# Kernel optimization log

Hardware: AMD Instinct MI355X
Metric: run time of the kernel (lower is better)

Reference implementation:

```python
import jax, jax.numpy as jnp
import numpy as np

B, T, D_IN, D_H, D_P = 256, 512, 256, 512, 512

def _lin(k, out_d, in_d):
    # torch nn.Linear default init: U(-1/sqrt(in_d), 1/sqrt(in_d))
    k1, k2 = jax.random.split(k)
    bound = 1.0 / np.sqrt(in_d)
    W = jax.random.uniform(k1, (out_d, in_d), jnp.float32, -bound, bound)
    b = jax.random.uniform(k2, (out_d,), jnp.float32, -bound, bound)
    return W, b

def setup_inputs() -> dict:
    key = jax.random.key(0)
    ks = jax.random.split(key, 8)
    x = jax.random.normal(ks[0], (B, T, D_IN), jnp.float32)
    # RNNCell params (torch init: U(-1/sqrt(hidden), 1/sqrt(hidden)) for all)
    bh = 1.0 / np.sqrt(D_H)
    k = jax.random.split(ks[1], 4)
    W_ih = jax.random.uniform(k[0], (D_H, D_IN), jnp.float32, -bh, bh)
    b_ih = jax.random.uniform(k[1], (D_H,), jnp.float32, -bh, bh)
    W_hh = jax.random.uniform(k[2], (D_H, D_H), jnp.float32, -bh, bh)
    b_hh = jax.random.uniform(k[3], (D_H,), jnp.float32, -bh, bh)
    W_ip, b_ip = _lin(ks[2], D_P, D_IN)
    W_hp, b_hp = _lin(ks[3], D_P, D_H)
    W_g, b_g = _lin(ks[4], D_P, D_IN + D_H)
    W_r, b_r = _lin(ks[5], D_P, D_P)
    W_o, b_o = _lin(ks[6], D_P, D_P)
    return dict(x=x, W_ih=W_ih, b_ih=b_ih, W_hh=W_hh, b_hh=b_hh,
                W_ip=W_ip, b_ip=b_ip, W_hp=W_hp, b_hp=b_hp,
                W_g=W_g, b_g=b_g, W_r=W_r, b_r=b_r, W_o=W_o, b_o=b_o)

def reference(x, W_ih, b_ih, W_hh, b_hh, W_ip, b_ip, W_hp, b_hp,
              W_g, b_g, W_r, b_r, W_o, b_o):
    batch = x.shape[0]
    # Precompute time-parallel projections of x outside the recurrence.
    x_ih = jnp.einsum('bti,hi->bth', x, W_ih) + b_ih + b_hh   # RNN input term
    x_proj_all = jnp.einsum('bti,pi->btp', x, W_ip) + b_ip
    # gate = sigmoid([x_t, h] @ W_g^T + b_g); split W_g into x-part and h-part
    W_gx, W_gh = W_g[:, :x.shape[-1]], W_g[:, x.shape[-1]:]
    gate_x_all = jnp.einsum('bti,pi->btp', x, W_gx) + b_g

    h0 = jnp.zeros((batch, W_hh.shape[0]), x.dtype)

    def step(h, inputs):
        x_ih_t, x_proj, gate_x = inputs
        h = jnp.tanh(x_ih_t + h @ W_hh.T)                # RNNCell (b_ih+b_hh folded in)
        h_proj = h @ W_hp.T + b_hp
        gate = jax.nn.sigmoid(gate_x + h @ W_gh.T)
        blended = gate * h_proj + (1.0 - gate) * x_proj
        res = blended @ W_r.T + b_r
        out_t = jax.nn.relu(res + blended)
        out_t = out_t @ W_o.T + b_o
        return h, out_t

    xs = (jnp.swapaxes(x_ih, 0, 1),       # (T, B, H)
          jnp.swapaxes(x_proj_all, 0, 1), # (T, B, P)
          jnp.swapaxes(gate_x_all, 0, 1)) # (T, B, P)
    _, outs = jax.lax.scan(step, h0, xs)
    return jnp.swapaxes(outs, 0, 1)       # (B, T, P)
```

## Files before the change

### kernel.cpp

```cpp
#include <hip/hip_runtime.h>
#include <hip/hip_bf16.h>
#include <cstdint>

#define RB   256
#define RT   512
#define ROWS (RB*RT)

typedef __attribute__((ext_vector_type(8))) short bf16x8;
typedef __attribute__((ext_vector_type(4))) short s16x4;
typedef __attribute__((ext_vector_type(4))) float f32x4;

#define DEV static __device__ __forceinline__

DEV float bf2f(unsigned short u){
  union { unsigned int i; float f; } v; v.i = ((unsigned int)u) << 16; return v.f;
}
DEV unsigned short f2bf(float f){
  union { float f; unsigned int i; } v; v.f = f;
  unsigned int x = v.i;
  return (unsigned short)((x + 0x7fffu + ((x >> 16) & 1u)) >> 16);
}
DEV float tanh_fast(float x){
  float xc = fminf(fmaxf(x, -15.f), 15.f);
  float e  = __expf(2.f * xc);
  return 1.f - 2.f * __builtin_amdgcn_rcpf(e + 1.f);
}
DEV float sigmoid_fast(float x){
  float xc = fminf(fmaxf(x, -30.f), 30.f);
  return __builtin_amdgcn_rcpf(1.f + __expf(-xc));
}
DEV void gl_lds16(const void* g, void* l){
  __builtin_amdgcn_global_load_lds(
      (const __attribute__((address_space(1))) unsigned int*)g,
      (__attribute__((address_space(3))) unsigned int*)l, 16, 0, 0);
}

struct ConvArgs {
  const float* src[15];
  unsigned short* dst[15];
  long pre[16];
};

__global__ __launch_bounds__(256) void conv_k(ConvArgs a, long total)
{
  long stride = (long)gridDim.x * blockDim.x;
  for (long idx = (long)blockIdx.x * blockDim.x + threadIdx.x; idx < total; idx += stride){
    int t = 0;
    #pragma unroll
    for (int j = 0; j < 14; j++) t += (idx >= a.pre[j + 1]) ? 1 : 0;
    long local = idx - a.pre[t];
    float4 v = ((const float4*)a.src[t])[local];
    s16x4 o;
    o[0] = (short)f2bf(v.x); o[1] = (short)f2bf(v.y);
    o[2] = (short)f2bf(v.z); o[3] = (short)f2bf(v.w);
    ((s16x4*)a.dst[t])[local] = o;
  }
}

__global__ __launch_bounds__(256, 2) void gemm_k(
    const unsigned short* __restrict__ A, int lda,
    const unsigned short* __restrict__ W, int ldb,
    const unsigned short* __restrict__ bias,
    const unsigned short* __restrict__ bias2,
    const unsigned short* __restrict__ addsrc,
    void* __restrict__ C,
    int K, int act, int out_f32)
{
  __shared__ unsigned short As[128*64];
  __shared__ unsigned short Bs[128*64];
  const int tid = threadIdx.x, w = tid >> 6, l = tid & 63;
  const int wm = w >> 1, wn = w & 1;
  const int lr = l & 15, lk = (l >> 4) * 8;
  const long row0 = (long)blockIdx.x * 128;
  const int  col0 = blockIdx.y * 128;

  f32x4 acc[4][4] = {};

  for (int k0 = 0; k0 < K; k0 += 64){
    __syncthreads();
    #pragma unroll
    for (int i = 0; i < 4; i++){
      int chunk = i*256 + tid;
      int r = chunk >> 3, kc = (chunk & 7) * 8;
      gl_lds16(A + (row0 + r)*lda + k0 + kc, (unsigned short*)As + (i*256 + w*64)*8);
      gl_lds16(W + (long)(col0 + r)*ldb + k0 + kc, (unsigned short*)Bs + (i*256 + w*64)*8);
    }
    asm volatile("s_waitcnt vmcnt(0)" ::: "memory");
    __syncthreads();
    #pragma unroll
    for (int ks = 0; ks < 2; ks++){
      bf16x8 a[4], b[4];
      #pragma unroll
      for (int mt = 0; mt < 4; mt++) a[mt] = *(const bf16x8*)&As[(wm*64 + mt*16 + lr)*64 + ks*32 + lk];
      #pragma unroll
      for (int nt = 0; nt < 4; nt++) b[nt] = *(const bf16x8*)&Bs[(wn*64 + nt*16 + lr)*64 + ks*32 + lk];
      #pragma unroll
      for (int mt = 0; mt < 4; mt++)
        #pragma unroll
        for (int nt = 0; nt < 4; nt++)
          acc[mt][nt] = __builtin_amdgcn_mfma_f32_16x16x32_bf16(a[mt], b[nt], acc[mt][nt], 0, 0, 0);
    }
  }

  #pragma unroll
  for (int nt = 0; nt < 4; nt++){
    int c = col0 + wn*64 + nt*16 + lr;
    float bv = bf2f(bias[c]);
    if (bias2) bv += bf2f(bias2[c]);
    #pragma unroll
    for (int mt = 0; mt < 4; mt++){
      #pragma unroll
      for (int i = 0; i < 4; i++){
        long r = row0 + wm*64 + mt*16 + (l >> 4)*4 + i;
        float v = acc[mt][nt][i] + bv;
        if (addsrc) v += bf2f(addsrc[r*512 + c]);
        if (act) v = fmaxf(v, 0.f);
        if (out_f32) ((float*)C)[r*512 + c] = v;
        else ((unsigned short*)C)[r*512 + c] = f2bf(v);
      }
    }
  }
}

__global__ __launch_bounds__(512, 2) void recur_k(
    const unsigned short* __restrict__ xih,
    const unsigned short* __restrict__ Whh,
    unsigned short* __restrict__ H)
{
  extern __shared__ unsigned short lds[];
  unsigned short* Wl = lds;
  unsigned short* hb = lds + 512*136;

  const int tid = threadIdx.x, w = tid >> 6, l = tid & 63;
  const int lr = l & 15, hi = l >> 4, lk = hi * 8;
  const int b0 = blockIdx.x * 16;
  const int cbase = w * 64;

  #pragma unroll
  for (int i = 0; i < 16; i++){
    int id = i*512 + tid;
    int c = id >> 4, j = (id & 15) * 8;
    *(bf16x8*)&Wl[c*136 + j] = *(const bf16x8*)&Whh[c*512 + 384 + j];
  }
  for (int i = tid; i < 16*520; i += 512) hb[i] = 0;

  bf16x8 wa[4][12];
  #pragma unroll
  for (int nt = 0; nt < 4; nt++){
    int c = cbase + nt*16 + lr;
    #pragma unroll
    for (int ks = 0; ks < 12; ks++)
      wa[nt][ks] = *(const bf16x8*)&Whh[c*512 + ks*32 + lk];
  }
  __syncthreads();

  const long xrow = ((long)(b0 + lr) * RT) * 512;

  for (int t = 0; t < RT; t++){
    uint2 xu[4];
    #pragma unroll
    for (int nt = 0; nt < 4; nt++)
      xu[nt] = *(const uint2*)&xih[xrow + (long)t*512 + cbase + nt*16 + hi*4];

    f32x4 acc[4] = {};
    #pragma unroll
    for (int ks = 0; ks < 16; ks++){
      bf16x8 hf = *(const bf16x8*)&hb[lr*520 + ks*32 + lk];
      #pragma unroll
      for (int nt = 0; nt < 4; nt++){
        bf16x8 af;
        if (ks < 12) af = wa[nt][ks];
        else         af = *(const bf16x8*)&Wl[(cbase + nt*16 + lr)*136 + (ks-12)*32 + lk];
        acc[nt] = __builtin_amdgcn_mfma_f32_16x16x32_bf16(af, hf, acc[nt], 0, 0, 0);
      }
    }

    unsigned int hv[4][2];
    #pragma unroll
    for (int nt = 0; nt < 4; nt++){
      float v0 = tanh_fast(acc[nt][0] + bf2f((unsigned short)(xu[nt].x & 0xffffu)));
      float v1 = tanh_fast(acc[nt][1] + bf2f((unsigned short)(xu[nt].x >> 16)));
      float v2 = tanh_fast(acc[nt][2] + bf2f((unsigned short)(xu[nt].y & 0xffffu)));
      float v3 = tanh_fast(acc[nt][3] + bf2f((unsigned short)(xu[nt].y >> 16)));
      hv[nt][0] = (unsigned)f2bf(v0) | ((unsigned)f2bf(v1) << 16);
      hv[nt][1] = (unsigned)f2bf(v2) | ((unsigned)f2bf(v3) << 16);
    }

    __syncthreads();
    #pragma unroll
    for (int nt = 0; nt < 4; nt++){
      uint2 p; p.x = hv[nt][0]; p.y = hv[nt][1];
      *(uint2*)&hb[lr*520 + cbase + nt*16 + hi*4] = p;
    }
    __syncthreads();

    {
      int r = tid >> 5, cb = (tid & 31) * 16;
      bf16x8 v0 = *(const bf16x8*)&hb[r*520 + cb];
      bf16x8 v1 = *(const bf16x8*)&hb[r*520 + cb + 8];
      long go = ((long)(b0 + r) * RT + t) * 512 + cb;
      *(bf16x8*)&H[go]     = v0;
      *(bf16x8*)&H[go + 8] = v1;
    }
  }
}

__global__ __launch_bounds__(256, 2) void blend_k(
    const unsigned short* __restrict__ X,
    const unsigned short* __restrict__ Hm,
    const unsigned short* __restrict__ Wg,
    const unsigned short* __restrict__ Wip,
    const unsigned short* __restrict__ Whp,
    const unsigned short* __restrict__ bg,
    const unsigned short* __restrict__ bip,
    const unsigned short* __restrict__ bhp,
    unsigned short* __restrict__ Out)
{
  __shared__ unsigned short As[128*64];
  __shared__ unsigned short Gs[128*64];
  __shared__ unsigned short Ps[128*64];
  const int tid = threadIdx.x, w = tid >> 6, l = tid & 63;
  const int wm = w >> 1, wn = w & 1;
  const int lr = l & 15, lk = (l >> 4) * 8;
  const long row0 = (long)blockIdx.x * 128;
  const int  col0 = blockIdx.y * 128;

  f32x4 accg[4][4] = {}, accp[4][4] = {};
  unsigned int xpp[4][4][2];

  #pragma unroll 1
  for (int k0 = 0; k0 < 768; k0 += 64){
    const bool ph1 = (k0 < 256);
    __syncthreads();
    #pragma unroll
    for (int i = 0; i < 4; i++){
      int chunk = i*256 + tid;
      int r = chunk >> 3, kc = (chunk & 7) * 8;
      const unsigned short* asrc = ph1 ? (X  + (row0 + r)*256 + k0 + kc)
                                       : (Hm + (row0 + r)*512 + (k0 - 256) + kc);
      gl_lds16(asrc, (unsigned short*)As + (i*256 + w*64)*8);
      gl_lds16(Wg + (long)(col0 + r)*768 + k0 + kc, (unsigned short*)Gs + (i*256 + w*64)*8);
      const unsigned short* psrc = ph1 ? (Wip + (col0 + r)*256 + k0 + kc)
                                       : (Whp + (col0 + r)*512 + (k0 - 256) + kc);
      gl_lds16(psrc, (unsigned short*)Ps + (i*256 + w*64)*8);
    }
    asm volatile("s_waitcnt vmcnt(0)" ::: "memory");
    __syncthreads();
    #pragma unroll
    for (int ks = 0; ks < 2; ks++){
      bf16x8 a[4], gq[4], pq[4];
      #pragma unroll
      for (int mt = 0; mt < 4; mt++) a[mt]  = *(const bf16x8*)&As[(wm*64 + mt*16 + lr)*64 + ks*32 + lk];
      #pragma unroll
      for (int nt = 0; nt < 4; nt++){
        gq[nt] = *(const bf16x8*)&Gs[(wn*64 + nt*16 + lr)*64 + ks*32 + lk];
        pq[nt] = *(const bf16x8*)&Ps[(wn*64 + nt*16 + lr)*64 + ks*32 + lk];
      }
      #pragma unroll
      for (int mt = 0; mt < 4; mt++)
        #pragma unroll
        for (int nt = 0; nt < 4; nt++){
          accg[mt][nt] = __builtin_amdgcn_mfma_f32_16x16x32_bf16(a[mt], gq[nt], accg[mt][nt], 0, 0, 0);
          accp[mt][nt] = __builtin_amdgcn_mfma_f32_16x16x32_bf16(a[mt], pq[nt], accp[mt][nt], 0, 0, 0);
        }
    }
    if (k0 == 192){
      #pragma unroll
      for (int mt = 0; mt < 4; mt++)
        #pragma unroll
        for (int nt = 0; nt < 4; nt++){
          xpp[mt][nt][0] = (unsigned)f2bf(accp[mt][nt][0]) | ((unsigned)f2bf(accp[mt][nt][1]) << 16);
          xpp[mt][nt][1] = (unsigned)f2bf(accp[mt][nt][2]) | ((unsigned)f2bf(accp[mt][nt][3]) << 16);
          accp[mt][nt] = (f32x4){0.f, 0.f, 0.f, 0.f};
        }
    }
  }

  #pragma unroll
  for (int nt = 0; nt < 4; nt++){
    int c = col0 + wn*64 + nt*16 + lr;
    float bgv = bf2f(bg[c]), bipv = bf2f(bip[c]), bhpv = bf2f(bhp[c]);
    #pragma unroll
    for (int mt = 0; mt < 4; mt++){
      #pragma unroll
      for (int i = 0; i < 4; i++){
        long r = row0 + wm*64 + mt*16 + (l >> 4)*4 + i;
        float g  = sigmoid_fast(accg[mt][nt][i] + bgv);
        float hp = accp[mt][nt][i] + bhpv;
        unsigned u = xpp[mt][nt][i >> 1];
        float xp = bf2f((unsigned short)((i & 1) ? (u >> 16) : (u & 0xffff))) + bipv;
        float v = g * hp + (1.f - g) * xp;
        Out[r*512 + c] = f2bf(v);
      }
    }
  }
}

extern "C" void kernel_launch(void* const* d_in, const int* in_sizes, int n_in,
                              void* d_out, int out_size, void* d_ws, size_t ws_size,
                              hipStream_t stream)
{
  static const long nelem[15] = {
    (long)ROWS*256,
    512*256, 512,
    512*512, 512,
    512*256, 512,
    512*512, 512,
    512*768, 512,
    512*512, 512,
    512*512, 512
  };

  unsigned char* ob = (unsigned char*)d_out;
  unsigned char* wb = (unsigned char*)d_ws;
  ConvArgs ca;
  long pre = 0;
  size_t doff = 0;
  for (int i = 0; i < 15; i++){
    ca.src[i] = (const float*)d_in[i];
    if (i == 13)      ca.dst[i] = (unsigned short*)(wb + 134217728u);
    else if (i == 14) ca.dst[i] = (unsigned short*)(wb + 134742016u);
    else              ca.dst[i] = (unsigned short*)(ob + doff);
    ca.pre[i] = pre;
    pre += nelem[i] / 4;
    if (i == 0) doff = 67108864u;
    else if (i < 13) doff += (size_t)nelem[i] * 2;
  }
  ca.pre[15] = pre;
  const long total_chunks = pre;

  const unsigned short* xb  = ca.dst[0];
  const unsigned short* Wih = ca.dst[1];
  const unsigned short* bih = ca.dst[2];
  const unsigned short* Whh = ca.dst[3];
  const unsigned short* bhh = ca.dst[4];
  const unsigned short* Wip = ca.dst[5];
  const unsigned short* bip = ca.dst[6];
  const unsigned short* Whp = ca.dst[7];
  const unsigned short* bhp = ca.dst[8];
  const unsigned short* Wg  = ca.dst[9];
  const unsigned short* bg  = ca.dst[10];
  const unsigned short* Wr  = ca.dst[11];
  const unsigned short* br  = ca.dst[12];
  const unsigned short* Wo  = ca.dst[13];
  const unsigned short* bo  = ca.dst[14];

  unsigned short* xih  = (unsigned short*)(ob + 75497472u);
  unsigned short* wsb  = (unsigned short*)d_ws;

  dim3 grid(ROWS / 128, 4), block(256);

  conv_k<<<2048, 256, 0, stream>>>(ca, total_chunks);

  gemm_k<<<grid, block, 0, stream>>>(xb, 256, Wih, 256, bih, bhh, nullptr, xih, 256, 0, 0);

  static const int kRecurLds = 512*136*2 + 16*520*2;
  hipFuncSetAttribute((const void*)recur_k, hipFuncAttributeMaxDynamicSharedMemorySize, kRecurLds);
  recur_k<<<16, 512, kRecurLds, stream>>>(xih, Whh, wsb);

  blend_k<<<grid, block, 0, stream>>>(xb, wsb, Wg, Wip, Whp, bg, bip, bhp, xih);

  gemm_k<<<grid, block, 0, stream>>>(xih, 512, Wr, 512, br, nullptr, xih, wsb, 512, 1, 0);

  gemm_k<<<grid, block, 0, stream>>>(wsb, 512, Wo, 512, bo, nullptr, nullptr, d_out, 512, 0, 1);
}
```

Measured before the change: 2.080 ms.

## Double-buffer RNN hidden state and stream W_hh tail from global memory

The recurrence kernel now keeps 10 of 16 W_hh k-slices in registers and streams the remaining 6 from a pre-swizzled global copy (built by a new wtail_k kernel). These loads are interleaved with the MFMAs as software-prefetched fragments instead of being held in a large LDS buffer. The hidden state is double-buffered in LDS, so one barrier per step replaces two, and H is written straight from registers rather than re-read from LDS. It also uses a packed bf16 convert instruction and drops the tanh input clamp, which risks inf/NaN handling for large inputs.

```diff
diff --git a/kernel.cpp b/kernel.cpp
--- a/kernel.cpp
+++ b/kernel.cpp
@@ -14,15 +14,25 @@
 
 DEV float bf2f(unsigned short u){
   union { unsigned int i; float f; } v; v.i = ((unsigned int)u) << 16; return v.f;
+}
+DEV float blo(unsigned int u){
+  union { unsigned int i; float f; } v; v.i = u << 16; return v.f;
+}
+DEV float bhi(unsigned int u){
+  union { unsigned int i; float f; } v; v.i = u & 0xffff0000u; return v.f;
 }
 DEV unsigned short f2bf(float f){
   union { float f; unsigned int i; } v; v.f = f;
   unsigned int x = v.i;
   return (unsigned short)((x + 0x7fffu + ((x >> 16) & 1u)) >> 16);
 }
+DEV unsigned int cvt_pk_bf16(float lo, float hi){
+  unsigned int r;
+  asm("v_cvt_pk_bf16_f32 %0, %1, %2" : "=v"(r) : "v"(lo), "v"(hi));
+  return r;
+}
 DEV float tanh_fast(float x){
-  float xc = fminf(fmaxf(x, -15.f), 15.f);
-  float e  = __expf(2.f * xc);
+  float e  = __expf(2.f * x);
   return 1.f - 2.f * __builtin_amdgcn_rcpf(e + 1.f);
 }
 DEV float sigmoid_fast(float x){
@@ -55,6 +65,20 @@
     o[2] = (short)f2bf(v.z); o[3] = (short)f2bf(v.w);
     ((s16x4*)a.dst[t])[local] = o;
   }
+}
+
+__global__ __launch_bounds__(256) void wtail_k(
+    const unsigned short* __restrict__ Whh, unsigned short* __restrict__ Wt)
+{
+  static const int kst[6] = {2, 5, 8, 11, 14, 15};
+  int id = blockIdx.x * 256 + threadIdx.x;
+  int l  = id & 63, fi = id >> 6;
+  int nt = fi & 3;
+  int k6 = (fi >> 2) % 6;
+  int w  = fi / 24;
+  int row = w*64 + nt*16 + (l & 15);
+  int col = kst[k6]*32 + (l >> 4)*8;
+  *(bf16x8*)&Wt[(long)id * 8] = *(const bf16x8*)&Whh[row*512 + col];
 }
 
 __global__ __launch_bounds__(256, 2) void gemm_k(
@@ -125,83 +149,113 @@
 __global__ __launch_bounds__(512, 2) void recur_k(
     const unsigned short* __restrict__ xih,
     const unsigned short* __restrict__ Whh,
+    const unsigned short* __restrict__ Wt,
     unsigned short* __restrict__ H)
 {
-  extern __shared__ unsigned short lds[];
-  unsigned short* Wl = lds;
-  unsigned short* hb = lds + 512*136;
+  __shared__ unsigned short hb[2][16*520];
 
   const int tid = threadIdx.x, w = tid >> 6, l = tid & 63;
   const int lr = l & 15, hi = l >> 4, lk = hi * 8;
   const int b0 = blockIdx.x * 16;
   const int cbase = w * 64;
 
-  #pragma unroll
-  for (int i = 0; i < 16; i++){
-    int id = i*512 + tid;
-    int c = id >> 4, j = (id & 15) * 8;
-    *(bf16x8*)&Wl[c*136 + j] = *(const bf16x8*)&Whh[c*512 + 384 + j];
-  }
-  for (int i = tid; i < 16*520; i += 512) hb[i] = 0;
-
-  bf16x8 wa[4][12];
+  static const int ksl[10] = {0, 1, 3, 4, 6, 7, 9, 10, 12, 13};
+  bf16x8 wa[4][10];
   #pragma unroll
   for (int nt = 0; nt < 4; nt++){
-    int c = cbase + nt*16 + lr;
-    #pragma unroll
-    for (int ks = 0; ks < 12; ks++)
-      wa[nt][ks] = *(const bf16x8*)&Whh[c*512 + ks*32 + lk];
-  }
+    const unsigned short* wp = Whh + (cbase + nt*16 + lr)*512 + lk;
+    #pragma unroll
+    for (int j = 0; j < 10; j++)
+      wa[nt][j] = *(const bf16x8*)&wp[ksl[j]*32];
+  }
+
+  for (int i = tid; i < 16*520; i += 512) hb[0][i] = 0;
+
+  const unsigned short* wtb = Wt + (long)w*12288 + l*8;
+
+  const unsigned short* h0 = &hb[0][lr*520 + lk];
+  const unsigned short* h1 = &hb[1][lr*520 + lk];
+  unsigned short* w0 = &hb[0][lr*520 + cbase + hi*4];
+  unsigned short* w1 = &hb[1][lr*520 + cbase + hi*4];
+
   __syncthreads();
 
-  const long xrow = ((long)(b0 + lr) * RT) * 512;
-
+  const long xbase = ((long)(b0 + lr) * RT) * 512 + cbase + hi*4;
+  const unsigned short* xr = xih + xbase;
+  unsigned short*       hr = H   + xbase;
+
+  int cur = 0;
   for (int t = 0; t < RT; t++){
+    const unsigned short* wtp;
+    { unsigned long long u = (unsigned long long)wtb;
+      asm volatile("" : "+v"(u));
+      wtp = (const unsigned short*)u; }
+
+    bf16x8 af0[4], af1[4];
+#define LG(A, K6) { const unsigned short* bp = wtp + (K6)*2048; \
+      A[0] = *(const bf16x8*)(bp);        A[1] = *(const bf16x8*)(bp + 512); \
+      A[2] = *(const bf16x8*)(bp + 1024); A[3] = *(const bf16x8*)(bp + 1536); }
+    LG(af0, 0);
+    LG(af1, 1);
+
     uint2 xu[4];
     #pragma unroll
     for (int nt = 0; nt < 4; nt++)
-      xu[nt] = *(const uint2*)&xih[xrow + (long)t*512 + cbase + nt*16 + hi*4];
-
+      xu[nt] = *(const uint2*)(xr + nt*16);
+
+    const unsigned short* hc = cur ? h1 : h0;
     f32x4 acc[4] = {};
-    #pragma unroll
-    for (int ks = 0; ks < 16; ks++){
-      bf16x8 hf = *(const bf16x8*)&hb[lr*520 + ks*32 + lk];
-      #pragma unroll
-      for (int nt = 0; nt < 4; nt++){
-        bf16x8 af;
-        if (ks < 12) af = wa[nt][ks];
-        else         af = *(const bf16x8*)&Wl[(cbase + nt*16 + lr)*136 + (ks-12)*32 + lk];
-        acc[nt] = __builtin_amdgcn_mfma_f32_16x16x32_bf16(af, hf, acc[nt], 0, 0, 0);
-      }
-    }
-
-    unsigned int hv[4][2];
+#define MM(A, K) { bf16x8 hf = *(const bf16x8*)(hc + (K)*32); \
+      acc[0] = __builtin_amdgcn_mfma_f32_16x16x32_bf16(A, hf, acc[0], 0, 0, 0); \
+      acc[1] = __builtin_amdgcn_mfma_f32_16x16x32_bf16(A##x, hf, acc[1], 0, 0, 0); }
+#define MR(J, K) { bf16x8 hf = *(const bf16x8*)(hc + (K)*32); \
+      acc[0] = __builtin_amdgcn_mfma_f32_16x16x32_bf16(wa[0][J], hf, acc[0], 0, 0, 0); \
+      acc[1] = __builtin_amdgcn_mfma_f32_16x16x32_bf16(wa[1][J], hf, acc[1], 0, 0, 0); \
+      acc[2] = __builtin_amdgcn_mfma_f32_16x16x32_bf16(wa[2][J], hf, acc[2], 0, 0, 0); \
+      acc[3] = __builtin_amdgcn_mfma_f32_16x16x32_bf16(wa[3][J], hf, acc[3], 0, 0, 0); }
+#define MG(A, K) { bf16x8 hf = *(const bf16x8*)(hc + (K)*32); \
+      acc[0] = __builtin_amdgcn_mfma_f32_16x16x32_bf16(A[0], hf, acc[0], 0, 0, 0); \
+      acc[1] = __builtin_amdgcn_mfma_f32_16x16x32_bf16(A[1], hf, acc[1], 0, 0, 0); \
+      acc[2] = __builtin_amdgcn_mfma_f32_16x16x32_bf16(A[2], hf, acc[2], 0, 0, 0); \
+      acc[3] = __builtin_amdgcn_mfma_f32_16x16x32_bf16(A[3], hf, acc[3], 0, 0, 0); }
+
+    MR(0, 0);  MR(1, 1);
+    MG(af0, 2);   LG(af0, 2);
+    MR(2, 3);  MR(3, 4);
+    MG(af1, 5);   LG(af1, 3);
+    MR(4, 6);  MR(5, 7);
+    MG(af0, 8);   LG(af0, 4);
+    MR(6, 9);  MR(7, 10);
+    MG(af1, 11);  LG(af1, 5);
+    MR(8, 12); MR(9, 13);
+    MG(af0, 14);
+    MG(af1, 15);
+#undef MR
+#undef MG
+#undef MM
+#undef LG
+
+    unsigned short* hw = cur ? w0 : w1;
+    uint2 P[4];
     #pragma unroll
     for (int nt = 0; nt < 4; nt++){
-      float v0 = tanh_fast(acc[nt][0] + bf2f((unsigned short)(xu[nt].x & 0xffffu)));
-      float v1 = tanh_fast(acc[nt][1] + bf2f((unsigned short)(xu[nt].x >> 16)));
-      float v2 = tanh_fast(acc[nt][2] + bf2f((unsigned short)(xu[nt].y & 0xffffu)));
-      float v3 = tanh_fast(acc[nt][3] + bf2f((unsigned short)(xu[nt].y >> 16)));
-      hv[nt][0] = (unsigned)f2bf(v0) | ((unsigned)f2bf(v1) << 16);
-      hv[nt][1] = (unsigned)f2bf(v2) | ((unsigned)f2bf(v3) << 16);
+      float v0 = tanh_fast(acc[nt][0] + blo(xu[nt].x));
+      float v1 = tanh_fast(acc[nt][1] + bhi(xu[nt].x));
+      float v2 = tanh_fast(acc[nt][2] + blo(xu[nt].y));
+      float v3 = tanh_fast(acc[nt][3] + bhi(xu[nt].y));
+      P[nt].x = cvt_pk_bf16(v0, v1);
+      P[nt].y = cvt_pk_bf16(v2, v3);
+      *(uint2*)(hw + nt*16) = P[nt];
     }
 
     __syncthreads();
-    #pragma unroll
-    for (int nt = 0; nt < 4; nt++){
-      uint2 p; p.x = hv[nt][0]; p.y = hv[nt][1];
-      *(uint2*)&hb[lr*520 + cbase + nt*16 + hi*4] = p;
-    }
-    __syncthreads();
-
-    {
-      int r = tid >> 5, cb = (tid & 31) * 16;
-      bf16x8 v0 = *(const bf16x8*)&hb[r*520 + cb];
-      bf16x8 v1 = *(const bf16x8*)&hb[r*520 + cb + 8];
-      long go = ((long)(b0 + r) * RT + t) * 512 + cb;
-      *(bf16x8*)&H[go]     = v0;
-      *(bf16x8*)&H[go + 8] = v1;
-    }
+
+    #pragma unroll
+    for (int nt = 0; nt < 4; nt++)
+      *(uint2*)(hr + nt*16) = P[nt];
+
+    xr += 512; hr += 512;
+    cur ^= 1;
   }
 }
 
@@ -346,17 +400,18 @@
   const unsigned short* bo  = ca.dst[14];
 
   unsigned short* xih  = (unsigned short*)(ob + 75497472u);
+  unsigned short* Wtl  = (unsigned short*)(ob + 209715200u);
   unsigned short* wsb  = (unsigned short*)d_ws;
 
   dim3 grid(ROWS / 128, 4), block(256);
 
   conv_k<<<2048, 256, 0, stream>>>(ca, total_chunks);
 
+  wtail_k<<<48, 256, 0, stream>>>(Whh, Wtl);
+
   gemm_k<<<grid, block, 0, stream>>>(xb, 256, Wih, 256, bih, bhh, nullptr, xih, 256, 0, 0);
 
-  static const int kRecurLds = 512*136*2 + 16*520*2;
-  hipFuncSetAttribute((const void*)recur_k, hipFuncAttributeMaxDynamicSharedMemorySize, kRecurLds);
-  recur_k<<<16, 512, kRecurLds, stream>>>(xih, Whh, wsb);
+  recur_k<<<16, 512, 0, stream>>>(xih, Whh, Wtl, wsb);
 
   blend_k<<<grid, block, 0, stream>>>(xb, wsb, Wg, Wip, Whp, bg, bip, bhp, xih);
 
```

New measurement: 3.172 ms. +52.5%, slower.

## Split recurrence across four workgroups per batch group with global flag sync

Applied to the files above, without the earlier changes.

The recurrence kernel now runs 64 workgroups instead of 16. Each batch group of 16 rows is split across four workgroups that each own 128 hidden columns and keep their W_hh slice in LDS in MFMA fragment order. The new h state is exchanged every timestep through a double-buffered global scratch area, with per-group step tags that are spin-polled, which replaces the block-local __syncthreads exchange. The aim is to cut per-step MFMA and LDS latency on the serial critical path by spreading it over more CUs. It adds cross-CU synchronisation latency each step and depends on all 64 workgroups being co-resident. Smaller changes also land: the tanh clamp is dropped, conversion uses packed v_cvt_pk_bf16, and the next x input is prefetched.

```diff
diff --git a/kernel.cpp b/kernel.cpp
--- a/kernel.cpp
+++ b/kernel.cpp
@@ -9,20 +9,31 @@
 typedef __attribute__((ext_vector_type(8))) short bf16x8;
 typedef __attribute__((ext_vector_type(4))) short s16x4;
 typedef __attribute__((ext_vector_type(4))) float f32x4;
+typedef unsigned long long ull;
 
 #define DEV static __device__ __forceinline__
 
 DEV float bf2f(unsigned short u){
   union { unsigned int i; float f; } v; v.i = ((unsigned int)u) << 16; return v.f;
+}
+DEV float blo(unsigned int u){
+  union { unsigned int i; float f; } v; v.i = u << 16; return v.f;
+}
+DEV float bhi(unsigned int u){
+  union { unsigned int i; float f; } v; v.i = u & 0xffff0000u; return v.f;
 }
 DEV unsigned short f2bf(float f){
   union { float f; unsigned int i; } v; v.f = f;
   unsigned int x = v.i;
   return (unsigned short)((x + 0x7fffu + ((x >> 16) & 1u)) >> 16);
 }
+DEV unsigned int cvt_pk_bf16(float lo, float hi){
+  unsigned int r;
+  asm("v_cvt_pk_bf16_f32 %0, %1, %2" : "=v"(r) : "v"(lo), "v"(hi));
+  return r;
+}
 DEV float tanh_fast(float x){
-  float xc = fminf(fmaxf(x, -15.f), 15.f);
-  float e  = __expf(2.f * xc);
+  float e  = __expf(2.f * x);
   return 1.f - 2.f * __builtin_amdgcn_rcpf(e + 1.f);
 }
 DEV float sigmoid_fast(float x){
@@ -41,8 +52,11 @@
   long pre[16];
 };
 
-__global__ __launch_bounds__(256) void conv_k(ConvArgs a, long total)
+__global__ __launch_bounds__(256) void conv_k(ConvArgs a, long total, unsigned int* tags)
 {
+  if (blockIdx.x == 0){
+    __hip_atomic_store(tags + threadIdx.x, 0u, __ATOMIC_RELAXED, __HIP_MEMORY_SCOPE_SYSTEM);
+  }
   long stride = (long)gridDim.x * blockDim.x;
   for (long idx = (long)blockIdx.x * blockDim.x + threadIdx.x; idx < total; idx += stride){
     int t = 0;
@@ -122,85 +136,108 @@
   }
 }
 
-__global__ __launch_bounds__(512, 2) void recur_k(
+__global__ __launch_bounds__(256, 1) void recur_k(
     const unsigned short* __restrict__ xih,
     const unsigned short* __restrict__ Whh,
-    unsigned short* __restrict__ H)
+    unsigned short* __restrict__ H,
+    ull* __restrict__ gx,
+    unsigned int* __restrict__ tags)
 {
-  extern __shared__ unsigned short lds[];
-  unsigned short* Wl = lds;
-  unsigned short* hb = lds + 512*136;
+  extern __shared__ unsigned short Wf[];
 
   const int tid = threadIdx.x, w = tid >> 6, l = tid & 63;
-  const int lr = l & 15, hi = l >> 4, lk = hi * 8;
-  const int b0 = blockIdx.x * 16;
-  const int cbase = w * 64;
+  const int lr = l & 15, hi = l >> 4;
+  const int g = blockIdx.x & 15, q = blockIdx.x >> 4;
+  const int b0 = g * 16;
 
   #pragma unroll
-  for (int i = 0; i < 16; i++){
-    int id = i*512 + tid;
-    int c = id >> 4, j = (id & 15) * 8;
-    *(bf16x8*)&Wl[c*136 + j] = *(const bf16x8*)&Whh[c*512 + 384 + j];
-  }
-  for (int i = tid; i < 16*520; i += 512) hb[i] = 0;
-
-  bf16x8 wa[4][12];
+  for (int i = 0; i < 32; i++){
+    int cid = i*256 + tid;
+    int fa = cid >> 6, ln = cid & 63;
+    int fw = fa >> 5, fnt = (fa >> 4) & 1, fks = fa & 15;
+    int row = q*128 + fw*32 + fnt*16 + (ln & 15);
+    int col = fks*32 + (ln >> 4)*8;
+    *(bf16x8*)&Wf[cid*8] = *(const bf16x8*)&Whh[row*512 + col];
+  }
+  __syncthreads();
+
+  const unsigned short* wf0 = Wf + (w*32 +  0)*512 + l*8;
+  const unsigned short* wf1 = Wf + (w*32 + 16)*512 + l*8;
+
+  const int colq = q*128 + w*32;
+  const long xb = ((long)(b0 + lr) * RT) * 512 + colq + hi*4;
+  const unsigned short* xr = xih + xb;
+  unsigned short*       hr = H   + xb;
+
+  const int fq = q*4 + w;
+  const int s0 = (((hi >> 1)     )*16 + lr)*2 + (hi & 1);
+  const int s1 = (((hi >> 1) + 2 )*16 + lr)*2 + (hi & 1);
+  unsigned int* tg = tags + g*16;
+
+  ull hfr[16][2];
   #pragma unroll
-  for (int nt = 0; nt < 4; nt++){
-    int c = cbase + nt*16 + lr;
-    #pragma unroll
-    for (int ks = 0; ks < 12; ks++)
-      wa[nt][ks] = *(const bf16x8*)&Whh[c*512 + ks*32 + lk];
-  }
-  __syncthreads();
-
-  const long xrow = ((long)(b0 + lr) * RT) * 512;
+  for (int ks = 0; ks < 16; ks++){ hfr[ks][0] = 0; hfr[ks][1] = 0; }
+
+  uint2 xu0 = *(const uint2*)(xr);
+  uint2 xu1 = *(const uint2*)(xr + 16);
 
   for (int t = 0; t < RT; t++){
-    uint2 xu[4];
-    #pragma unroll
-    for (int nt = 0; nt < 4; nt++)
-      xu[nt] = *(const uint2*)&xih[xrow + (long)t*512 + cbase + nt*16 + hi*4];
-
-    f32x4 acc[4] = {};
+    f32x4 acc0 = {}, acc1 = {};
     #pragma unroll
     for (int ks = 0; ks < 16; ks++){
-      bf16x8 hf = *(const bf16x8*)&hb[lr*520 + ks*32 + lk];
-      #pragma unroll
-      for (int nt = 0; nt < 4; nt++){
-        bf16x8 af;
-        if (ks < 12) af = wa[nt][ks];
-        else         af = *(const bf16x8*)&Wl[(cbase + nt*16 + lr)*136 + (ks-12)*32 + lk];
-        acc[nt] = __builtin_amdgcn_mfma_f32_16x16x32_bf16(af, hf, acc[nt], 0, 0, 0);
+      union { ull u[2]; bf16x8 v; } hv;
+      hv.u[0] = hfr[ks][0]; hv.u[1] = hfr[ks][1];
+      bf16x8 a0 = *(const bf16x8*)(wf0 + ks*512);
+      bf16x8 a1 = *(const bf16x8*)(wf1 + ks*512);
+      acc0 = __builtin_amdgcn_mfma_f32_16x16x32_bf16(a0, hv.v, acc0, 0, 0, 0);
+      acc1 = __builtin_amdgcn_mfma_f32_16x16x32_bf16(a1, hv.v, acc1, 0, 0, 0);
+    }
+
+    uint2 P0, P1;
+    {
+      float v0 = tanh_fast(acc0[0] + blo(xu0.x));
+      float v1 = tanh_fast(acc0[1] + bhi(xu0.x));
+      float v2 = tanh_fast(acc0[2] + blo(xu0.y));
+      float v3 = tanh_fast(acc0[3] + bhi(xu0.y));
+      P0.x = cvt_pk_bf16(v0, v1); P0.y = cvt_pk_bf16(v2, v3);
+      float u0 = tanh_fast(acc1[0] + blo(xu1.x));
+      float u1 = tanh_fast(acc1[1] + bhi(xu1.x));
+      float u2 = tanh_fast(acc1[2] + blo(xu1.y));
+      float u3 = tanh_fast(acc1[3] + bhi(xu1.y));
+      P1.x = cvt_pk_bf16(u0, u1); P1.y = cvt_pk_bf16(u2, u3);
+    }
+
+    ull* gb = gx + (size_t)((t & 1)*16 + g)*2048;
+    ull pk0 = (ull)P0.x | ((ull)P0.y << 32);
+    ull pk1 = (ull)P1.x | ((ull)P1.y << 32);
+    __hip_atomic_store(gb + fq*128 + s0, pk0, __ATOMIC_RELAXED, __HIP_MEMORY_SCOPE_SYSTEM);
+    __hip_atomic_store(gb + fq*128 + s1, pk1, __ATOMIC_RELAXED, __HIP_MEMORY_SCOPE_SYSTEM);
+    *(uint2*)(hr)      = P0;
+    *(uint2*)(hr + 16) = P1;
+    hr += 512;
+
+    if (t + 1 < RT){
+      xu0 = *(const uint2*)(xr + 512);
+      xu1 = *(const uint2*)(xr + 528);
+    }
+    xr += 512;
+
+    asm volatile("s_waitcnt vmcnt(0)" ::: "memory");
+
+    if (t + 1 < RT){
+      if (l == 0)
+        __hip_atomic_store(tg + fq, (unsigned)(t + 1), __ATOMIC_RELAXED, __HIP_MEMORY_SCOPE_SYSTEM);
+      const unsigned int* myp = tg + lr;
+      unsigned int mv;
+      do {
+        mv = __hip_atomic_load(myp, __ATOMIC_RELAXED, __HIP_MEMORY_SCOPE_SYSTEM);
+      } while (!__all((int)mv > t));
+      const ull* lb = gb + l*2;
+      #pragma unroll
+      for (int ks = 0; ks < 16; ks++){
+        hfr[ks][0] = __hip_atomic_load(lb + ks*128,     __ATOMIC_RELAXED, __HIP_MEMORY_SCOPE_SYSTEM);
+        hfr[ks][1] = __hip_atomic_load(lb + ks*128 + 1, __ATOMIC_RELAXED, __HIP_MEMORY_SCOPE_SYSTEM);
       }
-    }
-
-    unsigned int hv[4][2];
-    #pragma unroll
-    for (int nt = 0; nt < 4; nt++){
-      float v0 = tanh_fast(acc[nt][0] + bf2f((unsigned short)(xu[nt].x & 0xffffu)));
-      float v1 = tanh_fast(acc[nt][1] + bf2f((unsigned short)(xu[nt].x >> 16)));
-      float v2 = tanh_fast(acc[nt][2] + bf2f((unsigned short)(xu[nt].y & 0xffffu)));
-      float v3 = tanh_fast(acc[nt][3] + bf2f((unsigned short)(xu[nt].y >> 16)));
-      hv[nt][0] = (unsigned)f2bf(v0) | ((unsigned)f2bf(v1) << 16);
-      hv[nt][1] = (unsigned)f2bf(v2) | ((unsigned)f2bf(v3) << 16);
-    }
-
-    __syncthreads();
-    #pragma unroll
-    for (int nt = 0; nt < 4; nt++){
-      uint2 p; p.x = hv[nt][0]; p.y = hv[nt][1];
-      *(uint2*)&hb[lr*520 + cbase + nt*16 + hi*4] = p;
-    }
-    __syncthreads();
-
-    {
-      int r = tid >> 5, cb = (tid & 31) * 16;
-      bf16x8 v0 = *(const bf16x8*)&hb[r*520 + cb];
-      bf16x8 v1 = *(const bf16x8*)&hb[r*520 + cb + 8];
-      long go = ((long)(b0 + r) * RT + t) * 512 + cb;
-      *(bf16x8*)&H[go]     = v0;
-      *(bf16x8*)&H[go + 8] = v1;
     }
   }
 }
@@ -346,17 +383,19 @@
   const unsigned short* bo  = ca.dst[14];
 
   unsigned short* xih  = (unsigned short*)(ob + 75497472u);
+  ull*            gxb  = (ull*)(ob + 209715200u);
+  unsigned int*   tags = (unsigned int*)(ob + 210239488u);
   unsigned short* wsb  = (unsigned short*)d_ws;
 
   dim3 grid(ROWS / 128, 4), block(256);
 
-  conv_k<<<2048, 256, 0, stream>>>(ca, total_chunks);
+  conv_k<<<2048, 256, 0, stream>>>(ca, total_chunks, tags);
 
   gemm_k<<<grid, block, 0, stream>>>(xb, 256, Wih, 256, bih, bhh, nullptr, xih, 256, 0, 0);
 
-  static const int kRecurLds = 512*136*2 + 16*520*2;
+  static const int kRecurLds = 128 * 1024;
   hipFuncSetAttribute((const void*)recur_k, hipFuncAttributeMaxDynamicSharedMemorySize, kRecurLds);
-  recur_k<<<16, 512, kRecurLds, stream>>>(xih, Whh, wsb);
+  recur_k<<<64, 256, kRecurLds, stream>>>(xih, Whh, wsb, gxb, tags);
 
   blend_k<<<grid, block, 0, stream>>>(xb, wsb, Wg, Wip, Whp, bg, bip, bhp, xih);
 
```

Measured after the change: 3.137 ms. 50.8% more time.
